# Kernel tuning notes

Measured on AMD Instinct MI355X. Metric: run time of the kernel, lower is better.

## Reference

```python
import jax, jax.numpy as jnp
import numpy as np

B, S, D, H, E = 2, 1024, 1024, 4096, 8


def _xavier(key, shape):
    # matches torch.nn.init.xavier_uniform_ on a 3D tensor: fan_in/out from last two dims
    fan_in, fan_out = shape[-2], shape[-1]
    limit = float(np.sqrt(6.0 / (fan_in + fan_out)))
    return jax.random.uniform(key, shape, jnp.float32, -limit, limit)


def setup_inputs() -> dict:
    key = jax.random.key(0)
    ks = jax.random.split(key, 4)
    x = jax.random.normal(ks[0], (B, S, D), jnp.float32)
    router_w = jax.random.normal(ks[1], (D, E), jnp.float32) * (1.0 / np.sqrt(D))
    router_b = jnp.zeros((E,), jnp.float32)
    fc1_weight = _xavier(ks[2], (E, D, H))
    fc1_bias = jnp.zeros((E, H), jnp.float32)
    fc2_weight = _xavier(ks[3], (E, H, D))
    fc2_bias = jnp.zeros((E, D), jnp.float32)
    return {
        "x": x,
        "router_w": router_w,
        "router_b": router_b,
        "fc1_weight": fc1_weight,
        "fc1_bias": fc1_bias,
        "fc2_weight": fc2_weight,
        "fc2_bias": fc2_bias,
    }


def reference(x, router_w, router_b, fc1_weight, fc1_bias, fc2_weight, fc2_bias):
    b, s, d = x.shape
    x_flat = x.reshape(-1, d)                                  # [T, D]
    logits = x_flat @ router_w + router_b                       # [T, E]
    probs = jax.nn.softmax(logits, axis=-1)                     # [T, E]
    # per-expert FC1 + exact GELU (torch nn.GELU default is erf-based)
    h = jnp.einsum('td,edh->teh', x_flat, fc1_weight) + fc1_bias  # [T, E, H]
    h = jax.nn.gelu(h, approximate=False)
    expert_out = jnp.einsum('teh,ehd->ted', h, fc2_weight) + fc2_bias  # [T, E, D]
    out_flat = jnp.einsum('te,ted->td', probs, expert_out)      # [T, D]
    y = out_flat.reshape(b, s, d)
    router_probs = probs.reshape(b, s, -1)
    return y, router_probs
```

## Files before the change

### kernel.cpp

```cpp
#include <hip/hip_runtime.h>
#include <math.h>


typedef float f32x4 __attribute__((ext_vector_type(4)));
typedef __bf16 bf16x8 __attribute__((ext_vector_type(8)));

#define GLL16(gp, lp)                                                          \
  __builtin_amdgcn_global_load_lds(                                            \
      (const __attribute__((address_space(1))) void*)(gp),                     \
      (__attribute__((address_space(3))) void*)(lp), 16, 0, 0)

__device__ __forceinline__ float gelu_f(float h) {
  return 0.5f * h * (1.f + erff(h * 0.70710678118654752f));
}

__global__ void router_kernel(const float* __restrict__ x,
                              const float* __restrict__ rw,
                              const float* __restrict__ rb,
                              float* __restrict__ P,
                              float* __restrict__ probs_out)
{
  int gid = blockIdx.x * blockDim.x + threadIdx.x;
  int t = gid >> 6;
  int l = gid & 63;
  const float* xr = x + (size_t)t * 1024;
  float a[8];
#pragma unroll
  for (int e = 0; e < 8; ++e) a[e] = 0.f;
  for (int d = l; d < 1024; d += 64) {
    float xv = xr[d];
    f32x4 w0 = *(const f32x4*)(rw + d * 8);
    f32x4 w1 = *(const f32x4*)(rw + d * 8 + 4);
#pragma unroll
    for (int e = 0; e < 4; ++e) a[e] += xv * w0[e];
#pragma unroll
    for (int e = 0; e < 4; ++e) a[4 + e] += xv * w1[e];
  }
#pragma unroll
  for (int off = 32; off > 0; off >>= 1) {
#pragma unroll
    for (int e = 0; e < 8; ++e) a[e] += __shfl_down(a[e], off);
  }
  if (l == 0) {
#pragma unroll
    for (int e = 0; e < 8; ++e) a[e] += rb[e];
    float m = a[0];
#pragma unroll
    for (int e = 1; e < 8; ++e) m = fmaxf(m, a[e]);
    float s = 0.f;
#pragma unroll
    for (int e = 0; e < 8; ++e) { a[e] = __expf(a[e] - m); s += a[e]; }
    float inv = 1.f / s;
#pragma unroll
    for (int e = 0; e < 8; ++e) {
      float p = a[e] * inv;
      if (P) P[t * 8 + e] = p;
      probs_out[t * 8 + e] = p;
    }
  }
}

__global__ void cvt_kernel(const float* __restrict__ src,
                           __bf16* __restrict__ dst)
{
  size_t i = ((size_t)blockIdx.x * 256 + threadIdx.x) * 8;
  f32x4 v0 = *(const f32x4*)(src + i);
  f32x4 v1 = *(const f32x4*)(src + i + 4);
  bf16x8 o;
#pragma unroll
  for (int j = 0; j < 4; ++j) o[j] = (__bf16)v0[j];
#pragma unroll
  for (int j = 0; j < 4; ++j) o[4 + j] = (__bf16)v1[j];
  *(bf16x8*)(dst + i) = o;
}

__global__ void transconv_kernel(const float* __restrict__ src,
                                 __bf16* __restrict__ dst,
                                 int R, int C, int cChunk,
                                 size_t dstLd, size_t zOff)
{
  size_t bs = (size_t)blockIdx.z * (size_t)R * (size_t)C;
  size_t dzo = (size_t)blockIdx.z * zOff;
  int r = blockIdx.x * 256 + threadIdx.x;
  int c0 = blockIdx.y * cChunk;
  const float* s = src + bs + (size_t)r * C;
  for (int c = c0; c < c0 + cChunk; c += 8) {
    f32x4 v0 = *(const f32x4*)(s + c);
    f32x4 v1 = *(const f32x4*)(s + c + 4);
    float vv[8] = {v0[0], v0[1], v0[2], v0[3], v1[0], v1[1], v1[2], v1[3]};
#pragma unroll
    for (int j = 0; j < 8; ++j)
      dst[(size_t)(c + j) * dstLd + dzo + r] = (__bf16)vv[j];
  }
}

__device__ __forceinline__ void mfma_loop(const __bf16* A, const __bf16* B,
                                          int lda, int ldb, int K,
                                          __bf16* As, __bf16* Bs,
                                          f32x4 acc[4][4])
{
  const int tid = threadIdx.x;
  const int w = tid >> 6, l = tid & 63;
  const int sr = (w << 4) + (l >> 2);
  const int sc = (l & 3) << 4;
  const size_t ldaB = (size_t)lda * 2, ldbB = (size_t)ldb * 2;
  const char* Ab = (const char*)A + (size_t)sr * ldaB + sc;
  const char* Bb = (const char*)B + (size_t)sr * ldbB + sc;
  char* AsW = (char*)As + w * 1024;
  char* BsW = (char*)Bs + w * 1024;
  const int wm = w & 1, wn = w >> 1;
  const int fr = ((l & 15) * 32) + ((l >> 4) * 8);
  const __bf16* Af = As + wm * 2048 + fr;
  const __bf16* Bf = Bs + wn * 2048 + fr;

  for (int k0 = 0; k0 < K; k0 += 32) {
    __syncthreads();
    const size_t kB = (size_t)k0 * 2;
    GLL16(Ab + kB, AsW);
    GLL16(Ab + kB + 64 * ldaB, AsW + 4096);
    GLL16(Bb + kB, BsW);
    GLL16(Bb + kB + 64 * ldbB, BsW + 4096);
    __syncthreads();
    bf16x8 af[4], bfr[4];
#pragma unroll
    for (int i = 0; i < 4; ++i) af[i] = *(const bf16x8*)(Af + i * 512);
#pragma unroll
    for (int j = 0; j < 4; ++j) bfr[j] = *(const bf16x8*)(Bf + j * 512);
#pragma unroll
    for (int i = 0; i < 4; ++i)
#pragma unroll
      for (int j = 0; j < 4; ++j)
        acc[i][j] = __builtin_amdgcn_mfma_f32_16x16x32_bf16(af[i], bfr[j],
                                                            acc[i][j], 0, 0, 0);
  }
}

__global__ void gemm1_kernel(const __bf16* __restrict__ X,
                             const __bf16* __restrict__ W1T,
                             const float* __restrict__ b1,
                             const float* __restrict__ P,
                             __bf16* __restrict__ Hs,
                             int hs_ld, int e_off, size_t b_zstride)
{
  __shared__ __bf16 As[128 * 32], Bs[128 * 32];
  const int bm = blockIdx.x, bn = blockIdx.y, z = blockIdx.z;
  const int e = z + e_off;
  f32x4 acc[4][4];
  const f32x4 z4 = {0.f, 0.f, 0.f, 0.f};
#pragma unroll
  for (int i = 0; i < 4; ++i)
#pragma unroll
    for (int j = 0; j < 4; ++j) acc[i][j] = z4;

  const __bf16* A = X + (size_t)bm * 128 * 1024;
  const __bf16* B = W1T + (size_t)z * b_zstride + (size_t)bn * 128 * 1024;
  mfma_loop(A, B, 1024, 1024, 1024, As, Bs, acc);

  const int tid = threadIdx.x, w = tid >> 6, l = tid & 63;
  const int wm = w & 1, wn = w >> 1, q = l >> 4, c16 = l & 15;
  const int row0 = bm * 128 + wm * 64 + q * 4;
  const int col0 = bn * 128 + wn * 64 + c16;
  float b1v[4];
#pragma unroll
  for (int j = 0; j < 4; ++j)
    b1v[j] = b1[(size_t)e * 4096 + col0 + j * 16];
  float pv[4][4];
#pragma unroll
  for (int i = 0; i < 4; ++i)
#pragma unroll
    for (int r = 0; r < 4; ++r)
      pv[i][r] = P[(size_t)(row0 + i * 16 + r) * 8 + e];
  const int zcol = (hs_ld == 4096) ? 0 : z * 4096;
#pragma unroll
  for (int i = 0; i < 4; ++i)
#pragma unroll
    for (int j = 0; j < 4; ++j)
#pragma unroll
      for (int r = 0; r < 4; ++r) {
        float h = acc[i][j][r] + b1v[j];
        float o = gelu_f(h) * pv[i][r];
        Hs[(size_t)(row0 + i * 16 + r) * hs_ld + zcol + col0 + j * 16] =
            (__bf16)o;
      }
}

__global__ void gemm2_kernel(const __bf16* __restrict__ Hs,
                             const __bf16* __restrict__ W2T,
                             float* __restrict__ accb,
                             int lda, int ldb, int kz)
{
  __shared__ __bf16 As[128 * 32], Bs[128 * 32];
  const int bm = blockIdx.x, bn = blockIdx.y, z = blockIdx.z;
  f32x4 acc[4][4];
  const f32x4 z4 = {0.f, 0.f, 0.f, 0.f};
#pragma unroll
  for (int i = 0; i < 4; ++i)
#pragma unroll
    for (int j = 0; j < 4; ++j) acc[i][j] = z4;

  const __bf16* A = Hs + (size_t)bm * 128 * lda + (size_t)z * kz;
  const __bf16* B = W2T + (size_t)bn * 128 * ldb + (size_t)z * kz;
  mfma_loop(A, B, lda, ldb, 4096, As, Bs, acc);

  const int tid = threadIdx.x, w = tid >> 6, l = tid & 63;
  const int wm = w & 1, wn = w >> 1, q = l >> 4, c16 = l & 15;
  const int row0 = bm * 128 + wm * 64 + q * 4;
  const int col0 = bn * 128 + wn * 64 + c16;
#pragma unroll
  for (int i = 0; i < 4; ++i)
#pragma unroll
    for (int j = 0; j < 4; ++j)
#pragma unroll
      for (int r = 0; r < 4; ++r)
        unsafeAtomicAdd(
            accb + (size_t)(row0 + i * 16 + r) * 1024 + col0 + j * 16,
            acc[i][j][r]);
}

__global__ void finalize_kernel(const float* __restrict__ accb,
                                const float* __restrict__ P,
                                const float* __restrict__ b2,
                                float* __restrict__ y)
{
  int idx = blockIdx.x * 256 + threadIdx.x;
  int t = idx >> 8;
  int d0 = (idx & 255) << 2;
  f32x4 a = *(const f32x4*)(accb + (size_t)t * 1024 + d0);
#pragma unroll
  for (int e = 0; e < 8; ++e) {
    float p = P[t * 8 + e];
    f32x4 b = *(const f32x4*)(b2 + (size_t)e * 1024 + d0);
#pragma unroll
    for (int c = 0; c < 4; ++c) a[c] += p * b[c];
  }
  *(f32x4*)(y + (size_t)t * 1024 + d0) = a;
}

__global__ __launch_bounds__(256) void fused_naive_kernel(
    const float* __restrict__ x, const float* __restrict__ w1,
    const float* __restrict__ b1, const float* __restrict__ w2,
    const float* __restrict__ b2, const float* __restrict__ probs,
    float* __restrict__ y)
{
  __shared__ float xs[8][1024];
  __shared__ float gs[8][64];
  __shared__ float ps[8];
  const int tid = threadIdx.x;
  const int t0 = blockIdx.x * 8;
  const size_t DH = (size_t)1024 * 4096;
  const int tt = tid >> 5;
  const int d0 = (tid & 31) * 32;
  float acc[32];
#pragma unroll
  for (int i = 0; i < 32; ++i) acc[i] = 0.f;
  {
    const f32x4* xsrc = (const f32x4*)(x + (size_t)t0 * 1024);
    f32x4* xdst = (f32x4*)&xs[0][0];
    for (int i = tid; i < 2048; i += 256) xdst[i] = xsrc[i];
  }
  const int wv = tid >> 6;
  const int hl = tid & 63;
  for (int e = 0; e < 8; ++e) {
    if (tid < 8) ps[tid] = probs[(size_t)(t0 + tid) * 8 + e];
    __syncthreads();
    for (int hc = 0; hc < 4096; hc += 64) {
      float a0 = 0.f, a1 = 0.f;
      const float* w1p = w1 + (size_t)e * DH + hc + hl;
      for (int d = 0; d < 1024; ++d) {
        float wvv = w1p[(size_t)d * 4096];
        a0 += xs[wv * 2 + 0][d] * wvv;
        a1 += xs[wv * 2 + 1][d] * wvv;
      }
      __syncthreads();
      gs[wv * 2 + 0][hl] =
          ps[wv * 2 + 0] * gelu_f(a0 + b1[(size_t)e * 4096 + hc + hl]);
      gs[wv * 2 + 1][hl] =
          ps[wv * 2 + 1] * gelu_f(a1 + b1[(size_t)e * 4096 + hc + hl]);
      __syncthreads();
      const float* w2p = w2 + (size_t)e * DH + (size_t)hc * 1024 + d0;
      for (int hh = 0; hh < 64; ++hh) {
        float g = gs[tt][hh];
#pragma unroll
        for (int jb = 0; jb < 8; ++jb) {
          f32x4 w4 = *(const f32x4*)(w2p + (size_t)hh * 1024 + jb * 4);
#pragma unroll
          for (int j2 = 0; j2 < 4; ++j2) acc[jb * 4 + j2] += g * w4[j2];
        }
      }
    }
#pragma unroll
    for (int j = 0; j < 32; ++j)
      acc[j] += ps[tt] * b2[(size_t)e * 1024 + d0 + j];
    __syncthreads();
  }
  float* yp = y + (size_t)(t0 + tt) * 1024 + d0;
#pragma unroll
  for (int jb = 0; jb < 8; ++jb) {
    f32x4 o = {acc[jb * 4], acc[jb * 4 + 1], acc[jb * 4 + 2], acc[jb * 4 + 3]};
    *(f32x4*)(yp + jb * 4) = o;
  }
}

extern "C" void kernel_launch(void* const* d_in, const int* in_sizes, int n_in,
                              void* d_out, int out_size, void* d_ws,
                              size_t ws_size, hipStream_t stream)
{
  const float* x  = (const float*)d_in[0];
  const float* rw = (const float*)d_in[1];
  const float* rb = (const float*)d_in[2];
  const float* w1 = (const float*)d_in[3];
  const float* b1 = (const float*)d_in[4];
  const float* w2 = (const float*)d_in[5];
  const float* b2 = (const float*)d_in[6];
  float* y = (float*)d_out;
  float* probs_out = y + (size_t)2048 * 1024;

  const size_t DH = (size_t)1024 * 4096;
  const size_t BASE = (64 << 10) + (size_t)2048 * 1024 * 4 +
                      (size_t)2048 * 1024 * 2;
  const size_t TA = BASE + 8 * DH * 2 + (size_t)2048 * 32768 * 2;
  const size_t TB = BASE + DH * 2 + (size_t)2048 * 4096 * 2;

  char* ws = (char*)d_ws;
  float* P = (float*)ws;
  float* accb = (float*)(ws + (64 << 10));
  __bf16* xb = (__bf16*)(ws + (64 << 10) + (size_t)2048 * 1024 * 4);
  char* ws2 = ws + BASE;

  if (ws_size >= TA) {
    router_kernel<<<512, 256, 0, stream>>>(x, rw, rb, P, probs_out);
    hipMemsetAsync(accb, 0, (size_t)2048 * 1024 * 4, stream);
    cvt_kernel<<<1024, 256, 0, stream>>>(x, xb);
    __bf16* WT = (__bf16*)ws2;
    __bf16* Hs = WT + 8 * DH;
    transconv_kernel<<<dim3(4, 64, 8), 256, 0, stream>>>(
        w1, WT, 1024, 4096, 64, 1024, DH);
    gemm1_kernel<<<dim3(16, 32, 8), 256, 0, stream>>>(xb, WT, b1, P, Hs,
                                                      32768, 0, DH);
    transconv_kernel<<<dim3(16, 16, 8), 256, 0, stream>>>(
        w2, WT, 4096, 1024, 64, 32768, 4096);
    gemm2_kernel<<<dim3(16, 8, 8), 256, 0, stream>>>(Hs, WT, accb, 32768,
                                                     32768, 4096);
    finalize_kernel<<<2048, 256, 0, stream>>>(accb, P, b2, y);
  } else if (ws_size >= TB) {
    router_kernel<<<512, 256, 0, stream>>>(x, rw, rb, P, probs_out);
    hipMemsetAsync(accb, 0, (size_t)2048 * 1024 * 4, stream);
    cvt_kernel<<<1024, 256, 0, stream>>>(x, xb);
    __bf16* WT = (__bf16*)ws2;
    __bf16* HsE = WT + DH;
    for (int e = 0; e < 8; ++e) {
      transconv_kernel<<<dim3(4, 64, 1), 256, 0, stream>>>(
          w1 + e * DH, WT, 1024, 4096, 64, 1024, 0);
      gemm1_kernel<<<dim3(16, 32, 1), 256, 0, stream>>>(xb, WT, b1, P, HsE,
                                                        4096, e, 0);
      transconv_kernel<<<dim3(16, 16, 1), 256, 0, stream>>>(
          w2 + e * DH, WT, 4096, 1024, 64, 4096, 0);
      gemm2_kernel<<<dim3(16, 8, 1), 256, 0, stream>>>(HsE, WT, accb, 4096,
                                                       4096, 0);
    }
    finalize_kernel<<<2048, 256, 0, stream>>>(accb, P, b2, y);
  } else {
    router_kernel<<<512, 256, 0, stream>>>(x, rw, rb, (float*)nullptr,
                                           probs_out);
    fused_naive_kernel<<<256, 256, 0, stream>>>(x, w1, b1, w2, b2, probs_out,
                                                y);
  }
}
```

Before: 743.1 us.

## Double K-tile to 64 and XOR-swizzle LDS layout in MFMA GEMM loop

```diff
diff --git a/kernel.cpp b/kernel.cpp
--- a/kernel.cpp
+++ b/kernel.cpp
@@ -101,37 +101,45 @@
 {
   const int tid = threadIdx.x;
   const int w = tid >> 6, l = tid & 63;
-  const int sr = (w << 4) + (l >> 2);
-  const int sc = (l & 3) << 4;
+  const int rg = l >> 3;
+  const int csrc = ((l & 7) ^ rg) << 4;
   const size_t ldaB = (size_t)lda * 2, ldbB = (size_t)ldb * 2;
-  const char* Ab = (const char*)A + (size_t)sr * ldaB + sc;
-  const char* Bb = (const char*)B + (size_t)sr * ldbB + sc;
-  char* AsW = (char*)As + w * 1024;
-  char* BsW = (char*)Bs + w * 1024;
+  const char* Ab = (const char*)A + (size_t)(w * 32 + rg) * ldaB + csrc;
+  const char* Bb = (const char*)B + (size_t)(w * 32 + rg) * ldbB + csrc;
+  char* AsW = (char*)As + w * 4096;
+  char* BsW = (char*)Bs + w * 4096;
   const int wm = w & 1, wn = w >> 1;
-  const int fr = ((l & 15) * 32) + ((l >> 4) * 8);
-  const __bf16* Af = As + wm * 2048 + fr;
-  const __bf16* Bf = Bs + wn * 2048 + fr;
-
-  for (int k0 = 0; k0 < K; k0 += 32) {
+  const int m16 = l & 15, quad = l >> 4;
+  const int rowA0 = wm * 64 + m16;
+  const int rowB0 = wn * 64 + m16;
+  const int sw = m16 & 7;
+
+  for (int k0 = 0; k0 < K; k0 += 64) {
     __syncthreads();
     const size_t kB = (size_t)k0 * 2;
-    GLL16(Ab + kB, AsW);
-    GLL16(Ab + kB + 64 * ldaB, AsW + 4096);
-    GLL16(Bb + kB, BsW);
-    GLL16(Bb + kB + 64 * ldbB, BsW + 4096);
+#pragma unroll
+    for (int i = 0; i < 4; ++i) {
+      GLL16(Ab + kB + (size_t)(8 * i) * ldaB, AsW + i * 1024);
+      GLL16(Bb + kB + (size_t)(8 * i) * ldbB, BsW + i * 1024);
+    }
     __syncthreads();
-    bf16x8 af[4], bfr[4];
-#pragma unroll
-    for (int i = 0; i < 4; ++i) af[i] = *(const bf16x8*)(Af + i * 512);
-#pragma unroll
-    for (int j = 0; j < 4; ++j) bfr[j] = *(const bf16x8*)(Bf + j * 512);
-#pragma unroll
-    for (int i = 0; i < 4; ++i)
+#pragma unroll
+    for (int kk = 0; kk < 2; ++kk) {
+      const int pos = ((quad + 4 * kk) ^ sw) << 3;
+      bf16x8 af[4], bfr[4];
+#pragma unroll
+      for (int i = 0; i < 4; ++i)
+        af[i] = *(const bf16x8*)(As + (rowA0 + 16 * i) * 64 + pos);
 #pragma unroll
       for (int j = 0; j < 4; ++j)
-        acc[i][j] = __builtin_amdgcn_mfma_f32_16x16x32_bf16(af[i], bfr[j],
-                                                            acc[i][j], 0, 0, 0);
+        bfr[j] = *(const bf16x8*)(Bs + (rowB0 + 16 * j) * 64 + pos);
+#pragma unroll
+      for (int i = 0; i < 4; ++i)
+#pragma unroll
+        for (int j = 0; j < 4; ++j)
+          acc[i][j] = __builtin_amdgcn_mfma_f32_16x16x32_bf16(
+              af[i], bfr[j], acc[i][j], 0, 0, 0);
+    }
   }
 }
 
@@ -142,7 +150,7 @@
                              __bf16* __restrict__ Hs,
                              int hs_ld, int e_off, size_t b_zstride)
 {
-  __shared__ __bf16 As[128 * 32], Bs[128 * 32];
+  __shared__ __bf16 As[128 * 64], Bs[128 * 64];
   const int bm = blockIdx.x, bn = blockIdx.y, z = blockIdx.z;
   const int e = z + e_off;
   f32x4 acc[4][4];
@@ -189,7 +197,7 @@
                              float* __restrict__ accb,
                              int lda, int ldb, int kz)
 {
-  __shared__ __bf16 As[128 * 32], Bs[128 * 32];
+  __shared__ __bf16 As[128 * 64], Bs[128 * 64];
   const int bm = blockIdx.x, bn = blockIdx.y, z = blockIdx.z;
   f32x4 acc[4][4];
   const f32x4 z4 = {0.f, 0.f, 0.f, 0.f};
```

After: 709.4 us. -4.5%, faster.
